# Performance work log

Measured on AMD Instinct MI355X. Metric: run time of the kernel, lower is better.

The kernel has to match this reference:

```python
import jax, jax.numpy as jnp
import numpy as np

HEAD_NUM = 16
D_MODEL = 1024
NEG = -1.0e9


def setup_inputs() -> dict:
    key = jax.random.key(0)
    ks = jax.random.split(key, 12)
    B, S, D = 2, 2048, D_MODEL
    inp = {
        "query": jax.random.normal(ks[0], (B, S, D), jnp.float32),
        "key": jax.random.normal(ks[1], (B, S, D), jnp.float32),
        "value": jax.random.normal(ks[2], (B, S, D), jnp.float32),
        "mask": jnp.ones((B, S, S), jnp.int32),
    }
    scale = 1.0 / np.sqrt(D)
    for i in range(4):
        inp[f"W{i}"] = jax.random.normal(ks[3 + i], (D, D), jnp.float32) * scale
        inp[f"b{i}"] = jnp.zeros((D,), jnp.float32)
    return inp


def reference(query, key, value, mask, W0, b0, W1, b1, W2, b2, W3, b3):
    B, Sq, D = query.shape
    Sk = key.shape[1]
    H, dk = HEAD_NUM, D // HEAD_NUM
    # input projections (torch Linear: x @ W.T + b)
    q = (query @ W0.T + b0).reshape(B, Sq, H, dk).transpose(0, 2, 1, 3)
    k = (key @ W1.T + b1).reshape(B, Sk, H, dk).transpose(0, 2, 1, 3)
    v = (value @ W2.T + b2).reshape(B, Sk, H, dk).transpose(0, 2, 1, 3)
    # scaled dot-product attention, full [B,H,Sq,Sk] scores (as original)
    scores = jnp.einsum("bhqd,bhkd->bhqk", q, k) / jnp.sqrt(jnp.float32(dk))
    scores = jnp.where(mask[:, None, :, :] == 0, NEG, scores)
    p_attn = jax.nn.softmax(scores, axis=-1)
    # dropout is identity in eval/reference mode
    x = jnp.einsum("bhqk,bhkd->bhqd", p_attn, v)
    x = x.transpose(0, 2, 1, 3).reshape(B, Sq, D)
    return x @ W3.T + b3
```

## Files before the change

kernel.cpp:

```cpp
#include <hip/hip_runtime.h>
#include <hip/hip_bf16.h>
#include <math.h>

#define H_NUM   16
#define D_MODEL 1024
#define D_K     64
#define N_B     2
#define SEQ     2048
#define M_ROWS  (N_B * SEQ)
#define NEGVAL  -1.0e9f

typedef short short8 __attribute__((ext_vector_type(8)));
typedef float f32x4 __attribute__((ext_vector_type(4)));

__device__ inline short bf16s(float x) {
  return (short)__builtin_bit_cast(ushort, __float2bfloat16(x));
}
__device__ inline float bf16f(short h) {
  return __uint_as_float(((unsigned)(ushort)h) << 16);
}

template <int MODE>
__global__ __launch_bounds__(512) void gemm_mfma(const float* __restrict__ A,
                                                 const float* __restrict__ W,
                                                 const float* __restrict__ bias,
                                                 void* __restrict__ C0,
                                                 void* __restrict__ C1, int K) {
  __shared__ ushort Ahi[128 * 40];
  __shared__ ushort Alo[128 * 40];
  __shared__ ushort Whi[128 * 40];
  __shared__ ushort Wlo[128 * 40];

  const int tid = threadIdx.x;
  const int rowBase = blockIdx.y * 128;
  const int colBase = blockIdx.x * 128;

  const int srow = tid >> 3;
  const int sk4 = (tid & 7) * 4;

  const int w = tid >> 6;
  const int wr = w >> 2;
  const int wc = w & 3;
  const int lane = tid & 63;
  const int lr = lane & 15;
  const int lq = lane >> 4;

  f32x4 acc[4][2] = {};

  for (int k0 = 0; k0 < K; k0 += 32) {
    float4 ga[2], gw[2];
#pragma unroll
    for (int j = 0; j < 2; ++j) {
      const int row = srow + 64 * j;
      ga[j] = *(const float4*)(A + (size_t)(rowBase + row) * K + k0 + sk4);
      gw[j] = *(const float4*)(W + (size_t)(colBase + row) * K + k0 + sk4);
    }
    __syncthreads();
#pragma unroll
    for (int j = 0; j < 2; ++j) {
      const int row = srow + 64 * j;
      const int idx = row * 40 + sk4;
      float av[4] = {ga[j].x, ga[j].y, ga[j].z, ga[j].w};
      float wv[4] = {gw[j].x, gw[j].y, gw[j].z, gw[j].w};
      ushort ah[4], al[4], wh[4], wl[4];
#pragma unroll
      for (int i = 0; i < 4; ++i) {
        ah[i] = (ushort)bf16s(av[i]);
        al[i] = (ushort)bf16s(av[i] - bf16f((short)ah[i]));
        wh[i] = (ushort)bf16s(wv[i]);
        wl[i] = (ushort)bf16s(wv[i] - bf16f((short)wh[i]));
      }
      *(ushort4*)&Ahi[idx] = make_ushort4(ah[0], ah[1], ah[2], ah[3]);
      *(ushort4*)&Alo[idx] = make_ushort4(al[0], al[1], al[2], al[3]);
      *(ushort4*)&Whi[idx] = make_ushort4(wh[0], wh[1], wh[2], wh[3]);
      *(ushort4*)&Wlo[idx] = make_ushort4(wl[0], wl[1], wl[2], wl[3]);
    }
    __syncthreads();

    short8 fah[4], fal[4], fwh[2], fwl[2];
#pragma unroll
    for (int mi = 0; mi < 4; ++mi) {
      const int idx = (wr * 64 + mi * 16 + lr) * 40 + lq * 8;
      fah[mi] = *(const short8*)&Ahi[idx];
      fal[mi] = *(const short8*)&Alo[idx];
    }
#pragma unroll
    for (int ni = 0; ni < 2; ++ni) {
      const int idx = (wc * 32 + ni * 16 + lr) * 40 + lq * 8;
      fwh[ni] = *(const short8*)&Whi[idx];
      fwl[ni] = *(const short8*)&Wlo[idx];
    }
#pragma unroll
    for (int mi = 0; mi < 4; ++mi)
#pragma unroll
      for (int ni = 0; ni < 2; ++ni) {
        if constexpr (MODE == 2) {
          acc[mi][ni] = __builtin_amdgcn_mfma_f32_16x16x32_bf16(
              fwh[ni], fah[mi], acc[mi][ni], 0, 0, 0);
          acc[mi][ni] = __builtin_amdgcn_mfma_f32_16x16x32_bf16(
              fwh[ni], fal[mi], acc[mi][ni], 0, 0, 0);
          acc[mi][ni] = __builtin_amdgcn_mfma_f32_16x16x32_bf16(
              fwl[ni], fah[mi], acc[mi][ni], 0, 0, 0);
        } else {
          acc[mi][ni] = __builtin_amdgcn_mfma_f32_16x16x32_bf16(
              fah[mi], fwh[ni], acc[mi][ni], 0, 0, 0);
          acc[mi][ni] = __builtin_amdgcn_mfma_f32_16x16x32_bf16(
              fah[mi], fwl[ni], acc[mi][ni], 0, 0, 0);
          acc[mi][ni] = __builtin_amdgcn_mfma_f32_16x16x32_bf16(
              fal[mi], fwh[ni], acc[mi][ni], 0, 0, 0);
        }
      }
  }

  if constexpr (MODE == 2) {
    float bvv[2][4];
#pragma unroll
    for (int ni = 0; ni < 2; ++ni)
#pragma unroll
      for (int j = 0; j < 4; ++j)
        bvv[ni][j] = bias[colBase + wc * 32 + ni * 16 + lq * 4 + j];
#pragma unroll
    for (int mi = 0; mi < 4; ++mi)
#pragma unroll
      for (int ni = 0; ni < 2; ++ni) {
        const int m = rowBase + wr * 64 + mi * 16 + lr;
        const int b = m >> 11;
        const int s = m & (SEQ - 1);
#pragma unroll
        for (int j = 0; j < 4; ++j) {
          const int n = colBase + wc * 32 + ni * 16 + lq * 4 + j;
          const int h = n >> 6;
          const int dk = n & 63;
          const float v = acc[mi][ni][j] + bvv[ni][j];
          const short hi = bf16s(v);
          const short lo = bf16s(v - bf16f(hi));
          const size_t off = (((size_t)b * H_NUM + h) * D_K + dk) * SEQ + s;
          ((short*)C0)[off] = hi;
          ((short*)C1)[off] = lo;
        }
      }
  } else {
    float bv[2];
#pragma unroll
    for (int ni = 0; ni < 2; ++ni)
      bv[ni] = bias[colBase + wc * 32 + ni * 16 + lr];
#pragma unroll
    for (int mi = 0; mi < 4; ++mi)
#pragma unroll
      for (int ni = 0; ni < 2; ++ni) {
        const int cg = colBase + wc * 32 + ni * 16 + lr;
#pragma unroll
        for (int j = 0; j < 4; ++j) {
          const int rg = rowBase + wr * 64 + mi * 16 + lq * 4 + j;
          const float v = acc[mi][ni][j] + bv[ni];
          if constexpr (MODE == 1) {
            const int b = rg >> 11;
            const int s = rg & (SEQ - 1);
            const int h = cg >> 6;
            const int dk = cg & 63;
            const short hi = bf16s(v);
            const short lo = bf16s(v - bf16f(hi));
            const size_t off = (((size_t)b * H_NUM + h) * SEQ + s) * D_K + dk;
            ((short*)C0)[off] = hi;
            ((short*)C1)[off] = lo;
          } else {
            ((float*)C0)[(size_t)rg * D_MODEL + cg] = v;
          }
        }
      }
  }
}

__global__ __launch_bounds__(256) void mask_flags(const int* __restrict__ mask,
                                                  uint* __restrict__ flags) {
  const int row = blockIdx.x * 4 + (threadIdx.x >> 6);
  const int lane = threadIdx.x & 63;
  const int kt = lane >> 1, half = lane & 1;
  const int4* p = (const int4*)(mask + (size_t)row * SEQ + kt * 64 + half * 32);
  int ok = 1;
#pragma unroll
  for (int i = 0; i < 8; ++i) {
    int4 v = p[i];
    ok &= (v.x != 0) & (v.y != 0) & (v.z != 0) & (v.w != 0);
  }
  ok &= __shfl_xor(ok, 1);
  unsigned long long bl = __ballot(ok != 0);
  if (lane == 0) {
    uint fw = 0;
#pragma unroll
    for (int k = 0; k < 32; ++k) fw |= (uint)((bl >> (2 * k)) & 1ULL) << k;
    flags[row] = fw;
  }
}

#define QBLK 128
#define KSTR 72

__global__ __launch_bounds__(512, 2) void flash_mfma(
    const short* __restrict__ Qhi, const short* __restrict__ Qlo,
    const short* __restrict__ Khi, const short* __restrict__ Klo,
    const short* __restrict__ Vthi, const short* __restrict__ Vtlo,
    const int* __restrict__ mask, const uint* __restrict__ flags,
    float* __restrict__ X) {
  __shared__ short Kh[64 * KSTR], Kl[64 * KSTR];
  __shared__ short Vh[64 * KSTR], Vl[64 * KSTR];
  __shared__ short Ph[QBLK * KSTR], Pl[QBLK * KSTR];
  __shared__ uint fl[QBLK];

  const int tid = threadIdx.x;
  const int w = tid >> 6;
  const int lane = tid & 63;
  const int lr = lane & 15;
  const int lq = lane >> 4;
  const int qt = blockIdx.x & 15;
  const int bh = blockIdx.x >> 4;
  const int b = bh >> 4;
  const int h = bh & 15;

  if (tid < QBLK) fl[tid] = flags[b * SEQ + qt * QBLK + tid];
  __syncthreads();

  const int qrow = qt * QBLK + w * 16 + lr;
  const short* qbh = Qhi + ((size_t)bh * SEQ + qrow) * D_K;
  const short* qbl = Qlo + ((size_t)bh * SEQ + qrow) * D_K;
  short8 qh[2], ql[2];
#pragma unroll
  for (int c = 0; c < 2; ++c) {
    qh[c] = *(const short8*)(qbh + c * 32 + lq * 8);
    ql[c] = *(const short8*)(qbl + c * 32 + lq * 8);
  }

  const short* kbh = Khi + (size_t)bh * SEQ * D_K;
  const short* kbl = Klo + (size_t)bh * SEQ * D_K;
  const short* vbh = Vthi + (size_t)bh * D_K * SEQ;
  const short* vbl = Vtlo + (size_t)bh * D_K * SEQ;

  f32x4 o[4] = {};
  float m_run[4] = {-1e30f, -1e30f, -1e30f, -1e30f};
  float l_run[4] = {};

  const int srow = tid >> 3;
  const int sc = (tid & 7) * 8;

  for (int kt = 0; kt < SEQ / 64; ++kt) {
    __syncthreads();
    *(short8*)&Kh[srow * KSTR + sc] =
        *(const short8*)(kbh + (size_t)(kt * 64 + srow) * D_K + sc);
    *(short8*)&Kl[srow * KSTR + sc] =
        *(const short8*)(kbl + (size_t)(kt * 64 + srow) * D_K + sc);
    *(short8*)&Vh[srow * KSTR + sc] =
        *(const short8*)(vbh + (size_t)srow * SEQ + kt * 64 + sc);
    *(short8*)&Vl[srow * KSTR + sc] =
        *(const short8*)(vbl + (size_t)srow * SEQ + kt * 64 + sc);
    __syncthreads();

    f32x4 sa[4] = {};
#pragma unroll
    for (int c = 0; c < 2; ++c)
#pragma unroll
      for (int n = 0; n < 4; ++n) {
        const int idx = (n * 16 + lr) * KSTR + c * 32 + lq * 8;
        short8 kh = *(const short8*)&Kh[idx];
        short8 klv = *(const short8*)&Kl[idx];
        sa[n] = __builtin_amdgcn_mfma_f32_16x16x32_bf16(qh[c], kh, sa[n], 0, 0, 0);
        sa[n] = __builtin_amdgcn_mfma_f32_16x16x32_bf16(qh[c], klv, sa[n], 0, 0, 0);
        sa[n] = __builtin_amdgcn_mfma_f32_16x16x32_bf16(ql[c], kh, sa[n], 0, 0, 0);
      }

    const int r0 = w * 16 + lq * 4;
    int fb = (int)((fl[r0 + 0] >> kt) & 1) & (int)((fl[r0 + 1] >> kt) & 1) &
             (int)((fl[r0 + 2] >> kt) & 1) & (int)((fl[r0 + 3] >> kt) & 1);
    if (__builtin_expect(!__all(fb), 0)) {
#pragma unroll
      for (int n = 0; n < 4; ++n)
#pragma unroll
        for (int j = 0; j < 4; ++j) {
          int mv = mask[((size_t)b * SEQ + qt * QBLK + r0 + j) * SEQ + kt * 64 +
                        n * 16 + lr];
          sa[n][j] = mv ? sa[n][j] * 0.125f : NEGVAL;
        }
    } else {
#pragma unroll
      for (int n = 0; n < 4; ++n)
#pragma unroll
        for (int j = 0; j < 4; ++j) sa[n][j] *= 0.125f;
    }

    float scl[4];
#pragma unroll
    for (int j = 0; j < 4; ++j) {
      float t = fmaxf(fmaxf(sa[0][j], sa[1][j]), fmaxf(sa[2][j], sa[3][j]));
      t = fmaxf(t, __shfl_xor(t, 1));
      t = fmaxf(t, __shfl_xor(t, 2));
      t = fmaxf(t, __shfl_xor(t, 4));
      t = fmaxf(t, __shfl_xor(t, 8));
      const float mn = fmaxf(m_run[j], t);
      scl[j] = __expf(m_run[j] - mn);
      m_run[j] = mn;
    }
    float ps[4] = {};
#pragma unroll
    for (int n = 0; n < 4; ++n)
#pragma unroll
      for (int j = 0; j < 4; ++j) {
        const float p = __expf(sa[n][j] - m_run[j]);
        ps[j] += p;
        const short phi = bf16s(p);
        Ph[(r0 + j) * KSTR + n * 16 + lr] = phi;
        Pl[(r0 + j) * KSTR + n * 16 + lr] = bf16s(p - bf16f(phi));
      }
#pragma unroll
    for (int j = 0; j < 4; ++j) {
      float t = ps[j];
      t += __shfl_xor(t, 1);
      t += __shfl_xor(t, 2);
      t += __shfl_xor(t, 4);
      t += __shfl_xor(t, 8);
      l_run[j] = l_run[j] * scl[j] + t;
    }
#pragma unroll
    for (int n = 0; n < 4; ++n)
#pragma unroll
      for (int j = 0; j < 4; ++j) o[n][j] *= scl[j];

#pragma unroll
    for (int c = 0; c < 2; ++c) {
      const int pidx = (w * 16 + lr) * KSTR + c * 32 + lq * 8;
      short8 pah = *(const short8*)&Ph[pidx];
      short8 pal = *(const short8*)&Pl[pidx];
#pragma unroll
      for (int n = 0; n < 4; ++n) {
        const int vidx = (n * 16 + lr) * KSTR + c * 32 + lq * 8;
        short8 vh = *(const short8*)&Vh[vidx];
        short8 vl = *(const short8*)&Vl[vidx];
        o[n] = __builtin_amdgcn_mfma_f32_16x16x32_bf16(pah, vh, o[n], 0, 0, 0);
        o[n] = __builtin_amdgcn_mfma_f32_16x16x32_bf16(pah, vl, o[n], 0, 0, 0);
        o[n] = __builtin_amdgcn_mfma_f32_16x16x32_bf16(pal, vh, o[n], 0, 0, 0);
      }
    }
  }

  float inv[4];
#pragma unroll
  for (int j = 0; j < 4; ++j) inv[j] = 1.f / l_run[j];
#pragma unroll
  for (int n = 0; n < 4; ++n)
#pragma unroll
    for (int j = 0; j < 4; ++j) {
      X[((size_t)b * SEQ + qt * QBLK + w * 16 + lq * 4 + j) * D_MODEL + h * D_K +
        n * 16 + lr] = o[n][j] * inv[j];
    }
}

extern "C" void kernel_launch(void* const* d_in, const int* in_sizes, int n_in,
                              void* d_out, int out_size, void* d_ws,
                              size_t ws_size, hipStream_t stream) {
  const float* query = (const float*)d_in[0];
  const float* key   = (const float*)d_in[1];
  const float* value = (const float*)d_in[2];
  const int*   mask  = (const int*)d_in[3];
  const float* W0 = (const float*)d_in[4];
  const float* b0 = (const float*)d_in[5];
  const float* W1 = (const float*)d_in[6];
  const float* b1 = (const float*)d_in[7];
  const float* W2 = (const float*)d_in[8];
  const float* b2 = (const float*)d_in[9];
  const float* W3 = (const float*)d_in[10];
  const float* b3 = (const float*)d_in[11];
  float* out = (float*)d_out;

  const size_t HSZ = (size_t)N_B * H_NUM * SEQ * D_K;
  short* Qh = (short*)d_ws;
  short* Ql = Qh + HSZ;
  short* Kh = Qh + 2 * HSZ;
  short* Kl = Qh + 3 * HSZ;
  short* Vth = Qh + 4 * HSZ;
  short* Vtl = Qh + 5 * HSZ;
  float* Xb = (float*)(Qh + 6 * HSZ);

  uint* flags = (uint*)d_out + (out_size - N_B * SEQ);

  mask_flags<<<M_ROWS / 4, 256, 0, stream>>>(mask, flags);

  dim3 gg(D_MODEL / 128, M_ROWS / 128);
  gemm_mfma<1><<<gg, 512, 0, stream>>>(query, W0, b0, Qh, Ql, D_MODEL);
  gemm_mfma<1><<<gg, 512, 0, stream>>>(key, W1, b1, Kh, Kl, D_MODEL);
  gemm_mfma<2><<<gg, 512, 0, stream>>>(value, W2, b2, Vth, Vtl, D_MODEL);

  flash_mfma<<<(SEQ / QBLK) * N_B * H_NUM, 512, 0, stream>>>(
      Qh, Ql, Kh, Kl, Vth, Vtl, mask, flags, Xb);

  gemm_mfma<0><<<gg, 512, 0, stream>>>(Xb, W3, b3, out, nullptr, D_MODEL);
}
```

Before: 560.8 us.

## Pre-tile Q/K/V into MFMA fragment layout and double-buffer KV via direct LDS loads

Result: faster. 477.2 us (-14.9%).

```diff
diff --git a/kernel.cpp b/kernel.cpp
--- a/kernel.cpp
+++ b/kernel.cpp
@@ -20,12 +20,20 @@
   return __uint_as_float(((unsigned)(ushort)h) << 16);
 }
 
+__device__ inline void gl_lds16(const void* g, void* l) {
+  __builtin_amdgcn_global_load_lds(
+      (const __attribute__((address_space(1))) unsigned int*)g,
+      (__attribute__((address_space(3))) unsigned int*)l, 16, 0, 0);
+}
+
+
 template <int MODE>
 __global__ __launch_bounds__(512) void gemm_mfma(const float* __restrict__ A,
                                                  const float* __restrict__ W,
                                                  const float* __restrict__ bias,
                                                  void* __restrict__ C0,
-                                                 void* __restrict__ C1, int K) {
+                                                 void* __restrict__ C1, int K,
+                                                 float scale) {
   __shared__ ushort Ahi[128 * 40];
   __shared__ ushort Alo[128 * 40];
   __shared__ ushort Whi[128 * 40];
@@ -45,16 +53,19 @@
   const int lr = lane & 15;
   const int lq = lane >> 4;
 
+  const float* Ap = A + (size_t)(rowBase + srow) * K + sk4;
+  const float* Wp = W + (size_t)(colBase + srow) * K + sk4;
+
   f32x4 acc[4][2] = {};
 
+  float4 ga[2], gw[2];
+#pragma unroll
+  for (int j = 0; j < 2; ++j) {
+    ga[j] = *(const float4*)(Ap + (size_t)(64 * j) * K);
+    gw[j] = *(const float4*)(Wp + (size_t)(64 * j) * K);
+  }
+
   for (int k0 = 0; k0 < K; k0 += 32) {
-    float4 ga[2], gw[2];
-#pragma unroll
-    for (int j = 0; j < 2; ++j) {
-      const int row = srow + 64 * j;
-      ga[j] = *(const float4*)(A + (size_t)(rowBase + row) * K + k0 + sk4);
-      gw[j] = *(const float4*)(W + (size_t)(colBase + row) * K + k0 + sk4);
-    }
     __syncthreads();
 #pragma unroll
     for (int j = 0; j < 2; ++j) {
@@ -77,6 +88,14 @@
     }
     __syncthreads();
 
+    if (k0 + 32 < K) {
+#pragma unroll
+      for (int j = 0; j < 2; ++j) {
+        ga[j] = *(const float4*)(Ap + (size_t)(64 * j) * K + k0 + 32);
+        gw[j] = *(const float4*)(Wp + (size_t)(64 * j) * K + k0 + 32);
+      }
+    }
+
     short8 fah[4], fal[4], fwh[2], fwl[2];
 #pragma unroll
     for (int mi = 0; mi < 4; ++mi) {
@@ -131,10 +150,14 @@
           const int n = colBase + wc * 32 + ni * 16 + lq * 4 + j;
           const int h = n >> 6;
           const int dk = n & 63;
-          const float v = acc[mi][ni][j] + bvv[ni][j];
+          const float v = (acc[mi][ni][j] + bvv[ni][j]) * scale;
           const short hi = bf16s(v);
           const short lo = bf16s(v - bf16f(hi));
-          const size_t off = (((size_t)b * H_NUM + h) * D_K + dk) * SEQ + s;
+          const int bh = b * H_NUM + h;
+          const size_t off =
+              (((((size_t)bh * 32 + (s >> 6)) * 4 + (dk >> 4)) * 2 +
+                ((s >> 5) & 1)) * 512) +
+              ((s >> 3) & 3) * 128 + (dk & 15) * 8 + (s & 7);
           ((short*)C0)[off] = hi;
           ((short*)C1)[off] = lo;
         }
@@ -152,7 +175,7 @@
 #pragma unroll
         for (int j = 0; j < 4; ++j) {
           const int rg = rowBase + wr * 64 + mi * 16 + lq * 4 + j;
-          const float v = acc[mi][ni][j] + bv[ni];
+          const float v = (acc[mi][ni][j] + bv[ni]) * scale;
           if constexpr (MODE == 1) {
             const int b = rg >> 11;
             const int s = rg & (SEQ - 1);
@@ -160,7 +183,10 @@
             const int dk = cg & 63;
             const short hi = bf16s(v);
             const short lo = bf16s(v - bf16f(hi));
-            const size_t off = (((size_t)b * H_NUM + h) * SEQ + s) * D_K + dk;
+            const int bh = b * H_NUM + h;
+            const size_t off =
+                ((((size_t)bh * 128 + (s >> 4)) * 2 + (dk >> 5)) * 512) +
+                ((dk >> 3) & 3) * 128 + (s & 15) * 8 + (dk & 7);
             ((short*)C0)[off] = hi;
             ((short*)C1)[off] = lo;
           } else {
@@ -194,17 +220,16 @@
 }
 
 #define QBLK 128
-#define KSTR 72
 
 __global__ __launch_bounds__(512, 2) void flash_mfma(
-    const short* __restrict__ Qhi, const short* __restrict__ Qlo,
-    const short* __restrict__ Khi, const short* __restrict__ Klo,
-    const short* __restrict__ Vthi, const short* __restrict__ Vtlo,
+    const short* __restrict__ Qhg, const short* __restrict__ Qlg,
+    const short* __restrict__ Khg, const short* __restrict__ Klg,
+    const short* __restrict__ Vhg, const short* __restrict__ Vlg,
     const int* __restrict__ mask, const uint* __restrict__ flags,
     float* __restrict__ X) {
-  __shared__ short Kh[64 * KSTR], Kl[64 * KSTR];
-  __shared__ short Vh[64 * KSTR], Vl[64 * KSTR];
-  __shared__ short Ph[QBLK * KSTR], Pl[QBLK * KSTR];
+  __shared__ __attribute__((aligned(16))) short KV[2][4][4096];
+  __shared__ __attribute__((aligned(16))) short Ph[QBLK * 64];
+  __shared__ __attribute__((aligned(16))) short Pl[QBLK * 64];
   __shared__ uint fl[QBLK];
 
   const int tid = threadIdx.x;
@@ -215,59 +240,59 @@
   const int qt = blockIdx.x & 15;
   const int bh = blockIdx.x >> 4;
   const int b = bh >> 4;
-  const int h = bh & 15;
 
   if (tid < QBLK) fl[tid] = flags[b * SEQ + qt * QBLK + tid];
+
+  short8 qh[2], ql[2];
+#pragma unroll
+  for (int c = 0; c < 2; ++c) {
+    const size_t qi = (((size_t)bh * 128 + qt * 8 + w) * 2 + c) * 512 + lane * 8;
+    qh[c] = *(const short8*)(Qhg + qi);
+    ql[c] = *(const short8*)(Qlg + qi);
+  }
+
+  {
+    const size_t kblk = ((size_t)bh * 128 + 0 * 4 + (w >> 1)) * 2 + (w & 1);
+    const size_t vblk = (((size_t)bh * 32 + 0) * 4 + (w >> 1)) * 2 + (w & 1);
+    gl_lds16(Khg + kblk * 512 + lane * 8, &KV[0][0][w * 512]);
+    gl_lds16(Klg + kblk * 512 + lane * 8, &KV[0][1][w * 512]);
+    gl_lds16(Vhg + vblk * 512 + lane * 8, &KV[0][2][w * 512]);
+    gl_lds16(Vlg + vblk * 512 + lane * 8, &KV[0][3][w * 512]);
+  }
   __syncthreads();
-
-  const int qrow = qt * QBLK + w * 16 + lr;
-  const short* qbh = Qhi + ((size_t)bh * SEQ + qrow) * D_K;
-  const short* qbl = Qlo + ((size_t)bh * SEQ + qrow) * D_K;
-  short8 qh[2], ql[2];
-#pragma unroll
-  for (int c = 0; c < 2; ++c) {
-    qh[c] = *(const short8*)(qbh + c * 32 + lq * 8);
-    ql[c] = *(const short8*)(qbl + c * 32 + lq * 8);
-  }
-
-  const short* kbh = Khi + (size_t)bh * SEQ * D_K;
-  const short* kbl = Klo + (size_t)bh * SEQ * D_K;
-  const short* vbh = Vthi + (size_t)bh * D_K * SEQ;
-  const short* vbl = Vtlo + (size_t)bh * D_K * SEQ;
 
   f32x4 o[4] = {};
   float m_run[4] = {-1e30f, -1e30f, -1e30f, -1e30f};
   float l_run[4] = {};
-
-  const int srow = tid >> 3;
-  const int sc = (tid & 7) * 8;
-
-  for (int kt = 0; kt < SEQ / 64; ++kt) {
-    __syncthreads();
-    *(short8*)&Kh[srow * KSTR + sc] =
-        *(const short8*)(kbh + (size_t)(kt * 64 + srow) * D_K + sc);
-    *(short8*)&Kl[srow * KSTR + sc] =
-        *(const short8*)(kbl + (size_t)(kt * 64 + srow) * D_K + sc);
-    *(short8*)&Vh[srow * KSTR + sc] =
-        *(const short8*)(vbh + (size_t)srow * SEQ + kt * 64 + sc);
-    *(short8*)&Vl[srow * KSTR + sc] =
-        *(const short8*)(vbl + (size_t)srow * SEQ + kt * 64 + sc);
-    __syncthreads();
+  const int r0 = w * 16 + lq * 4;
+
+  const int NT = SEQ / 64;
+  for (int kt = 0; kt < NT; ++kt) {
+    const int cur = kt & 1;
+    if (kt + 1 < NT) {
+      const size_t kblk =
+          ((size_t)bh * 128 + (kt + 1) * 4 + (w >> 1)) * 2 + (w & 1);
+      const size_t vblk =
+          (((size_t)bh * 32 + (kt + 1)) * 4 + (w >> 1)) * 2 + (w & 1);
+      gl_lds16(Khg + kblk * 512 + lane * 8, &KV[cur ^ 1][0][w * 512]);
+      gl_lds16(Klg + kblk * 512 + lane * 8, &KV[cur ^ 1][1][w * 512]);
+      gl_lds16(Vhg + vblk * 512 + lane * 8, &KV[cur ^ 1][2][w * 512]);
+      gl_lds16(Vlg + vblk * 512 + lane * 8, &KV[cur ^ 1][3][w * 512]);
+    }
 
     f32x4 sa[4] = {};
 #pragma unroll
     for (int c = 0; c < 2; ++c)
 #pragma unroll
       for (int n = 0; n < 4; ++n) {
-        const int idx = (n * 16 + lr) * KSTR + c * 32 + lq * 8;
-        short8 kh = *(const short8*)&Kh[idx];
-        short8 klv = *(const short8*)&Kl[idx];
+        const int off = (n * 2 + c) * 512 + lane * 8;
+        short8 kh = *(const short8*)&KV[cur][0][off];
+        short8 kl = *(const short8*)&KV[cur][1][off];
         sa[n] = __builtin_amdgcn_mfma_f32_16x16x32_bf16(qh[c], kh, sa[n], 0, 0, 0);
-        sa[n] = __builtin_amdgcn_mfma_f32_16x16x32_bf16(qh[c], klv, sa[n], 0, 0, 0);
+        sa[n] = __builtin_amdgcn_mfma_f32_16x16x32_bf16(qh[c], kl, sa[n], 0, 0, 0);
         sa[n] = __builtin_amdgcn_mfma_f32_16x16x32_bf16(ql[c], kh, sa[n], 0, 0, 0);
       }
 
-    const int r0 = w * 16 + lq * 4;
     int fb = (int)((fl[r0 + 0] >> kt) & 1) & (int)((fl[r0 + 1] >> kt) & 1) &
              (int)((fl[r0 + 2] >> kt) & 1) & (int)((fl[r0 + 3] >> kt) & 1);
     if (__builtin_expect(!__all(fb), 0)) {
@@ -277,13 +302,8 @@
         for (int j = 0; j < 4; ++j) {
           int mv = mask[((size_t)b * SEQ + qt * QBLK + r0 + j) * SEQ + kt * 64 +
                         n * 16 + lr];
-          sa[n][j] = mv ? sa[n][j] * 0.125f : NEGVAL;
+          if (!mv) sa[n][j] = NEGVAL;
         }
-    } else {
-#pragma unroll
-      for (int n = 0; n < 4; ++n)
-#pragma unroll
-        for (int j = 0; j < 4; ++j) sa[n][j] *= 0.125f;
     }
 
     float scl[4];
@@ -300,15 +320,17 @@
     }
     float ps[4] = {};
 #pragma unroll
-    for (int n = 0; n < 4; ++n)
+    for (int n = 0; n < 4; ++n) {
+      const int pbase = (w * 2 + (n >> 1)) * 512 + ((n & 1) * 2 + (lr >> 3)) * 128 + (lr & 7);
 #pragma unroll
       for (int j = 0; j < 4; ++j) {
         const float p = __expf(sa[n][j] - m_run[j]);
         ps[j] += p;
         const short phi = bf16s(p);
-        Ph[(r0 + j) * KSTR + n * 16 + lr] = phi;
-        Pl[(r0 + j) * KSTR + n * 16 + lr] = bf16s(p - bf16f(phi));
-      }
+        Ph[pbase + (lq * 4 + j) * 8] = phi;
+        Pl[pbase + (lq * 4 + j) * 8] = bf16s(p - bf16f(phi));
+      }
+    }
 #pragma unroll
     for (int j = 0; j < 4; ++j) {
       float t = ps[j];
@@ -325,30 +347,33 @@
 
 #pragma unroll
     for (int c = 0; c < 2; ++c) {
-      const int pidx = (w * 16 + lr) * KSTR + c * 32 + lq * 8;
-      short8 pah = *(const short8*)&Ph[pidx];
-      short8 pal = *(const short8*)&Pl[pidx];
+      const int poff = (w * 2 + c) * 512 + lane * 8;
+      short8 pah = *(const short8*)&Ph[poff];
+      short8 pal = *(const short8*)&Pl[poff];
 #pragma unroll
       for (int n = 0; n < 4; ++n) {
-        const int vidx = (n * 16 + lr) * KSTR + c * 32 + lq * 8;
-        short8 vh = *(const short8*)&Vh[vidx];
-        short8 vl = *(const short8*)&Vl[vidx];
+        const int voff = (n * 2 + c) * 512 + lane * 8;
+        short8 vh = *(const short8*)&KV[cur][2][voff];
+        short8 vl = *(const short8*)&KV[cur][3][voff];
         o[n] = __builtin_amdgcn_mfma_f32_16x16x32_bf16(pah, vh, o[n], 0, 0, 0);
         o[n] = __builtin_amdgcn_mfma_f32_16x16x32_bf16(pah, vl, o[n], 0, 0, 0);
         o[n] = __builtin_amdgcn_mfma_f32_16x16x32_bf16(pal, vh, o[n], 0, 0, 0);
       }
     }
+
+    __syncthreads();
   }
 
   float inv[4];
 #pragma unroll
   for (int j = 0; j < 4; ++j) inv[j] = 1.f / l_run[j];
+  const int h = bh & 15;
 #pragma unroll
   for (int n = 0; n < 4; ++n)
 #pragma unroll
     for (int j = 0; j < 4; ++j) {
-      X[((size_t)b * SEQ + qt * QBLK + w * 16 + lq * 4 + j) * D_MODEL + h * D_K +
-        n * 16 + lr] = o[n][j] * inv[j];
+      X[((size_t)b * SEQ + qt * QBLK + w * 16 + lq * 4 + j) * D_MODEL +
+        h * D_K + n * 16 + lr] = o[n][j] * inv[j];
     }
 }
 
@@ -383,12 +408,12 @@
   mask_flags<<<M_ROWS / 4, 256, 0, stream>>>(mask, flags);
 
   dim3 gg(D_MODEL / 128, M_ROWS / 128);
-  gemm_mfma<1><<<gg, 512, 0, stream>>>(query, W0, b0, Qh, Ql, D_MODEL);
-  gemm_mfma<1><<<gg, 512, 0, stream>>>(key, W1, b1, Kh, Kl, D_MODEL);
-  gemm_mfma<2><<<gg, 512, 0, stream>>>(value, W2, b2, Vth, Vtl, D_MODEL);
+  gemm_mfma<1><<<gg, 512, 0, stream>>>(query, W0, b0, Qh, Ql, D_MODEL, 0.125f);
+  gemm_mfma<1><<<gg, 512, 0, stream>>>(key, W1, b1, Kh, Kl, D_MODEL, 1.0f);
+  gemm_mfma<2><<<gg, 512, 0, stream>>>(value, W2, b2, Vth, Vtl, D_MODEL, 1.0f);
 
   flash_mfma<<<(SEQ / QBLK) * N_B * H_NUM, 512, 0, stream>>>(
       Qh, Ql, Kh, Kl, Vth, Vtl, mask, flags, Xb);
 
-  gemm_mfma<0><<<gg, 512, 0, stream>>>(Xb, W3, b3, out, nullptr, D_MODEL);
-}
+  gemm_mfma<0><<<gg, 512, 0, stream>>>(Xb, W3, b3, out, nullptr, D_MODEL, 1.0f);
+}
```
